# Optimization experiments

Measured on AMD Instinct MI355X. Metric: run time of the kernel, lower is better.

The kernel has to match this reference:

```python
import jax, jax.numpy as jnp
import numpy as np

B = 65536
G = 9          # grid_size
C = 10         # num_classes
BS = 3         # block_size = sqrt(grid_size)
CONSTRAINT_WEIGHT = 0.1


def setup_inputs() -> dict:
    key = jax.random.key(0)
    k1, k2, k3 = jax.random.split(key, 3)
    logits = jax.random.normal(k1, (B, G, G, C), dtype=jnp.float32)
    targets = jax.random.randint(k2, (B, G, G), 0, C)
    puzzles = jax.random.randint(k3, (B, G, G), 0, C)
    return {"logits": logits, "targets": targets, "puzzles": puzzles}


def _sudoku_loss(logits, targets, puzzles):
    mask = (puzzles == 0).astype(logits.dtype)               # [B, G, G]

    # --- masked cross-entropy over empty cells ---
    logp = jax.nn.log_softmax(logits, axis=-1)               # [B, G, G, C]
    ce = -jnp.take_along_axis(logp, targets[..., None], axis=-1)[..., 0]
    ce_loss = (ce * mask).sum() / (mask.sum() + 1e-8)

    # --- constraint loss (rows, cols, 3x3 boxes), fully vectorized ---
    probs = jnp.exp(logp)                                    # softmax probs
    wp = probs * mask[..., None]                             # [B, G, G, C]

    def group_mse(digit_sums, msum):
        # digit_sums: [B, G_groups, C]; msum: [B, G_groups]
        # torch: per-group F.mse_loss over [B, C-1], summed over groups
        target = msum[..., None] / G                         # [B, Gg, 1]
        diff = digit_sums[..., 1:] - target                  # [B, Gg, C-1]
        return (diff * diff).mean(axis=(0, 2)).sum()

    # rows: sum over columns (axis 2)
    row_loss = group_mse(wp.sum(axis=2), mask.sum(axis=2))
    # cols: sum over rows (axis 1)
    col_loss = group_mse(wp.sum(axis=1), mask.sum(axis=1))
    # boxes: reshape to [B, bi, ri, bj, cj, C], sum within-box dims
    box_ds = wp.reshape(B, BS, BS, BS, BS, C).sum(axis=(2, 4)).reshape(B, G, C)
    box_ms = mask.reshape(B, BS, BS, BS, BS).sum(axis=(2, 4)).reshape(B, G)
    box_loss = group_mse(box_ds, box_ms)

    num_constraints = G * 2 + BS * BS                        # 27
    constraint_loss = (row_loss + col_loss + box_loss) / num_constraints

    # torch wraps the constraint loss in torch.tensor(...), detaching it
    total = ce_loss + CONSTRAINT_WEIGHT * jax.lax.stop_gradient(constraint_loss)
    return total, ce_loss, constraint_loss


def reference(logits, targets, puzzles):
    total, ce_loss, constraint_loss = _sudoku_loss(logits, targets, puzzles)
    return total, ce_loss, constraint_loss
```

## Files before the change

kernel.cpp:

```cpp
#include <hip/hip_runtime.h>


constexpr int kB = 65536;
constexpr int kPuzzPerBlk = 3;
constexpr int kBlocks = (kB + kPuzzPerBlk - 1) / kPuzzPerBlk;

__global__ __launch_bounds__(256) void sudoku_main(
    const float* __restrict__ logits,
    const int*   __restrict__ targets,
    const int*   __restrict__ puzzles,
    float*       __restrict__ ws)
{
    __shared__ float acc[kPuzzPerBlk][27][10];
    __shared__ float red[4][3];

    const int tid = threadIdx.x;
    for (int i = tid; i < kPuzzPerBlk * 270; i += 256) ((float*)acc)[i] = 0.f;
    __syncthreads();

    float ce = 0.f, mcnt = 0.f, diff2 = 0.f;

    const int q    = tid / 81;
    const int cell = tid - q * 81;
    const int p    = blockIdx.x * kPuzzPerBlk + q;
    const bool valid = (tid < 243) && (p < kB);

    if (valid) {
        const size_t base = (size_t)p * 81 + cell;
        const int pz = puzzles[base];
        if (pz == 0) {
            const int t = targets[base];
            const float* xp = logits + base * 10;
            float x[10];
            #pragma unroll
            for (int h = 0; h < 5; ++h) {
                const float2 v = *(const float2*)(xp + 2 * h);
                x[2 * h] = v.x; x[2 * h + 1] = v.y;
            }
            float mx = x[0];
            #pragma unroll
            for (int c = 1; c < 10; ++c) mx = fmaxf(mx, x[c]);
            float e[10], S = 0.f;
            #pragma unroll
            for (int c = 0; c < 10; ++c) { e[c] = __expf(x[c] - mx); S += e[c]; }
            const float inv = 1.f / S;
            const float lse = __logf(S);

            float xt = x[0];
            #pragma unroll
            for (int c = 1; c < 10; ++c) xt = (t == c) ? x[c] : xt;
            ce   += mx + lse - xt;
            mcnt += 1.f;

            const int r  = cell / 9;
            const int cj = cell - r * 9;
            const int bx = (r / 3) * 3 + (cj / 3);
            float* rowa = acc[q][r];
            float* cola = acc[q][9 + cj];
            float* boxa = acc[q][18 + bx];
            atomicAdd(&rowa[0], 1.f);
            atomicAdd(&cola[0], 1.f);
            atomicAdd(&boxa[0], 1.f);
            #pragma unroll
            for (int c = 1; c < 10; ++c) {
                const float w = e[c] * inv;
                atomicAdd(&rowa[c], w);
                atomicAdd(&cola[c], w);
                atomicAdd(&boxa[c], w);
            }
        }
    }
    __syncthreads();

    if (tid < kPuzzPerBlk * 27) {
        const int q2 = tid / 27;
        const int g  = tid - q2 * 27;
        if (blockIdx.x * kPuzzPerBlk + q2 < kB) {
            const float* a = acc[q2][g];
            const float tg = a[0] * (1.f / 9.f);
            #pragma unroll
            for (int c = 1; c < 10; ++c) { const float d = a[c] - tg; diff2 += d * d; }
        }
    }

    #pragma unroll
    for (int off = 32; off > 0; off >>= 1) {
        diff2 += __shfl_down(diff2, off);
        ce    += __shfl_down(ce, off);
        mcnt  += __shfl_down(mcnt, off);
    }
    const int wave = tid >> 6;
    const int lane = tid & 63;
    if (lane == 0) { red[wave][0] = diff2; red[wave][1] = ce; red[wave][2] = mcnt; }
    __syncthreads();
    if (tid == 0) {
        float d = 0.f, c2 = 0.f, m = 0.f;
        #pragma unroll
        for (int wv = 0; wv < 4; ++wv) { d += red[wv][0]; c2 += red[wv][1]; m += red[wv][2]; }
        const int b = blockIdx.x;
        ws[b]               = d;
        ws[kBlocks + b]     = c2;
        ws[2 * kBlocks + b] = m;
    }
}

__global__ __launch_bounds__(1024) void sudoku_final(
    const float* __restrict__ ws, float* __restrict__ out)
{
    __shared__ float red[16][3];
    float s0 = 0.f, s1 = 0.f, s2 = 0.f;
    for (int i = threadIdx.x; i < kBlocks; i += 1024) {
        s0 += ws[i];
        s1 += ws[kBlocks + i];
        s2 += ws[2 * kBlocks + i];
    }
    #pragma unroll
    for (int off = 32; off > 0; off >>= 1) {
        s0 += __shfl_down(s0, off);
        s1 += __shfl_down(s1, off);
        s2 += __shfl_down(s2, off);
    }
    const int wave = threadIdx.x >> 6;
    if ((threadIdx.x & 63) == 0) { red[wave][0] = s0; red[wave][1] = s1; red[wave][2] = s2; }
    __syncthreads();
    if (threadIdx.x == 0) {
        float d = 0.f, c2 = 0.f, m = 0.f;
        #pragma unroll
        for (int wv = 0; wv < 16; ++wv) { d += red[wv][0]; c2 += red[wv][1]; m += red[wv][2]; }
        const float ce_loss    = c2 / (m + 1e-8f);
        const float constraint = d / ((float)kB * 9.f * 27.f);
        out[0] = ce_loss + 0.1f * constraint;
        out[1] = ce_loss;
        out[2] = constraint;
    }
}

extern "C" void kernel_launch(void* const* d_in, const int* in_sizes, int n_in,
                              void* d_out, int out_size, void* d_ws, size_t ws_size,
                              hipStream_t stream)
{
    const float* logits  = (const float*)d_in[0];
    const int*   targets = (const int*)d_in[1];
    const int*   puzzles = (const int*)d_in[2];
    float* ws  = (float*)d_ws;
    float* out = (float*)d_out;

    sudoku_main<<<kBlocks, 256, 0, stream>>>(logits, targets, puzzles, ws);
    sudoku_final<<<1, 1024, 0, stream>>>(ws, out);
}
```

Measured before the change: 369.1 us.

## Persistent tiled blocks with coalesced staging and masked-cell compaction

Replaces one-block-per-3-puzzles with 1024 persistent blocks that each loop over 8-puzzle tiles. Puzzles and targets are staged into shared memory with int4 loads, and logits are copied with float4 loads only where an empty cell is touched. Each wave builds a ballot-compacted worklist of empty cells so lanes stay busy. This aims to cut uncoalesced float2 global reads and skip loading logits for filled cells, at the cost of more barriers per tile and extra shared-memory traffic.

```diff
diff --git a/kernel.cpp b/kernel.cpp
--- a/kernel.cpp
+++ b/kernel.cpp
@@ -1,9 +1,13 @@
 #include <hip/hip_runtime.h>
 
 
-constexpr int kB = 65536;
-constexpr int kPuzzPerBlk = 3;
-constexpr int kBlocks = (kB + kPuzzPerBlk - 1) / kPuzzPerBlk;
+constexpr int kB            = 65536;
+constexpr int kPuzzPerTile  = 8;
+constexpr int kCellsPerTile = kPuzzPerTile * 81;
+constexpr int kFloatsPerTile= kCellsPerTile * 10;
+constexpr int kVec4PerTile  = kFloatsPerTile / 4;
+constexpr int kBlocks       = 1024;
+constexpr int kTilesPerBlk  = kB / (kBlocks * kPuzzPerTile);
 
 __global__ __launch_bounds__(256) void sudoku_main(
     const float* __restrict__ logits,
@@ -11,26 +15,64 @@
     const int*   __restrict__ puzzles,
     float*       __restrict__ ws)
 {
-    __shared__ float acc[kPuzzPerBlk][27][10];
-    __shared__ float red[4][3];
+    __shared__ float         lgs[kFloatsPerTile];
+    __shared__ unsigned char pzs[kCellsPerTile];
+    __shared__ int           tgs[kCellsPerTile];
+    __shared__ float         acc[kPuzzPerTile][27][10];
+    __shared__ unsigned short wl[4][164];
+    __shared__ float         red[4][3];
 
-    const int tid = threadIdx.x;
-    for (int i = tid; i < kPuzzPerBlk * 270; i += 256) ((float*)acc)[i] = 0.f;
-    __syncthreads();
+    const int tid  = threadIdx.x;
+    const int wave = tid >> 6;
+    const int lane = tid & 63;
 
-    float ce = 0.f, mcnt = 0.f, diff2 = 0.f;
+    for (int i = tid; i < kPuzzPerTile * 270; i += 256) ((float*)acc)[i] = 0.f;
 
-    const int q    = tid / 81;
-    const int cell = tid - q * 81;
-    const int p    = blockIdx.x * kPuzzPerBlk + q;
-    const bool valid = (tid < 243) && (p < kB);
+    float diff2 = 0.f, ce = 0.f, mcnt = 0.f;
 
-    if (valid) {
-        const size_t base = (size_t)p * 81 + cell;
-        const int pz = puzzles[base];
-        if (pz == 0) {
-            const int t = targets[base];
-            const float* xp = logits + base * 10;
+    for (int it = 0; it < kTilesPerBlk; ++it) {
+        const size_t tile     = (size_t)blockIdx.x * kTilesPerBlk + it;
+        const size_t cellBase = tile * kCellsPerTile;
+
+        if (tid < kCellsPerTile / 4) {
+            const int4 v = ((const int4*)(puzzles + cellBase))[tid];
+            unsigned char* p = &pzs[4 * tid];
+            p[0] = (unsigned char)v.x; p[1] = (unsigned char)v.y;
+            p[2] = (unsigned char)v.z; p[3] = (unsigned char)v.w;
+            ((int4*)tgs)[tid] = ((const int4*)(targets + cellBase))[tid];
+        }
+        __syncthreads();
+
+        {
+            const float4* lg4 = (const float4*)(logits + cellBase * 10);
+            #pragma unroll
+            for (int k = tid; k < kVec4PerTile; k += 256) {
+                const int f0 = 4 * k;
+                const int c0 = f0 / 10;
+                const int c1 = (f0 + 3) / 10;
+                if ((pzs[c0] == 0) || (pzs[c1] == 0))
+                    ((float4*)lgs)[k] = lg4[k];
+            }
+        }
+
+        int wcount = 0;
+        {
+            const int wbase = wave * 162;
+            #pragma unroll
+            for (int rb = 0; rb < 162; rb += 64) {
+                const int ci = rb + lane;
+                const bool m = (ci < 162) && (pzs[wbase + ci] == 0);
+                const unsigned long long bal = __ballot(m);
+                const int pre = __popcll(bal & ((1ULL << lane) - 1ULL));
+                if (m) wl[wave][wcount + pre] = (unsigned short)(wbase + ci);
+                wcount += (int)__popcll(bal);
+            }
+        }
+        __syncthreads();
+
+        for (int i = lane; i < wcount; i += 64) {
+            const int cid = wl[wave][i];
+            const float* xp = &lgs[cid * 10];
             float x[10];
             #pragma unroll
             for (int h = 0; h < 5; ++h) {
@@ -46,18 +88,22 @@
             const float inv = 1.f / S;
             const float lse = __logf(S);
 
+            const int t = tgs[cid];
             float xt = x[0];
             #pragma unroll
             for (int c = 1; c < 10; ++c) xt = (t == c) ? x[c] : xt;
             ce   += mx + lse - xt;
             mcnt += 1.f;
 
-            const int r  = cell / 9;
-            const int cj = cell - r * 9;
-            const int bx = (r / 3) * 3 + (cj / 3);
-            float* rowa = acc[q][r];
-            float* cola = acc[q][9 + cj];
-            float* boxa = acc[q][18 + bx];
+            const int q    = cid / 81;
+            const int cell = cid - q * 81;
+            const int r    = cell / 9;
+            const int cj   = cell - r * 9;
+            const int bx   = (r / 3) * 3 + (cj / 3);
+            float* A = &acc[q][0][0];
+            float* rowa = A + r * 10;
+            float* cola = A + (9 + cj) * 10;
+            float* boxa = A + (18 + bx) * 10;
             atomicAdd(&rowa[0], 1.f);
             atomicAdd(&cola[0], 1.f);
             atomicAdd(&boxa[0], 1.f);
@@ -69,18 +115,19 @@
                 atomicAdd(&boxa[c], w);
             }
         }
-    }
-    __syncthreads();
+        __syncthreads();
 
-    if (tid < kPuzzPerBlk * 27) {
-        const int q2 = tid / 27;
-        const int g  = tid - q2 * 27;
-        if (blockIdx.x * kPuzzPerBlk + q2 < kB) {
-            const float* a = acc[q2][g];
+        if (tid < kPuzzPerTile * 27) {
+            const int q = tid / 27;
+            const int g = tid - q * 27;
+            float* a = &acc[q][g][0];
             const float tg = a[0] * (1.f / 9.f);
             #pragma unroll
             for (int c = 1; c < 10; ++c) { const float d = a[c] - tg; diff2 += d * d; }
+            #pragma unroll
+            for (int c = 0; c < 10; ++c) a[c] = 0.f;
         }
+        __syncthreads();
     }
 
     #pragma unroll
@@ -89,8 +136,6 @@
         ce    += __shfl_down(ce, off);
         mcnt  += __shfl_down(mcnt, off);
     }
-    const int wave = tid >> 6;
-    const int lane = tid & 63;
     if (lane == 0) { red[wave][0] = diff2; red[wave][1] = ce; red[wave][2] = mcnt; }
     __syncthreads();
     if (tid == 0) {
@@ -98,18 +143,18 @@
         #pragma unroll
         for (int wv = 0; wv < 4; ++wv) { d += red[wv][0]; c2 += red[wv][1]; m += red[wv][2]; }
         const int b = blockIdx.x;
-        ws[b]               = d;
-        ws[kBlocks + b]     = c2;
-        ws[2 * kBlocks + b] = m;
+        ws[b]                = d;
+        ws[kBlocks + b]      = c2;
+        ws[2 * kBlocks + b]  = m;
     }
 }
 
-__global__ __launch_bounds__(1024) void sudoku_final(
+__global__ __launch_bounds__(256) void sudoku_final(
     const float* __restrict__ ws, float* __restrict__ out)
 {
-    __shared__ float red[16][3];
+    __shared__ float red[4][3];
     float s0 = 0.f, s1 = 0.f, s2 = 0.f;
-    for (int i = threadIdx.x; i < kBlocks; i += 1024) {
+    for (int i = threadIdx.x; i < kBlocks; i += 256) {
         s0 += ws[i];
         s1 += ws[kBlocks + i];
         s2 += ws[2 * kBlocks + i];
@@ -126,7 +171,7 @@
     if (threadIdx.x == 0) {
         float d = 0.f, c2 = 0.f, m = 0.f;
         #pragma unroll
-        for (int wv = 0; wv < 16; ++wv) { d += red[wv][0]; c2 += red[wv][1]; m += red[wv][2]; }
+        for (int wv = 0; wv < 4; ++wv) { d += red[wv][0]; c2 += red[wv][1]; m += red[wv][2]; }
         const float ce_loss    = c2 / (m + 1e-8f);
         const float constraint = d / ((float)kB * 9.f * 27.f);
         out[0] = ce_loss + 0.1f * constraint;
@@ -146,5 +191,5 @@
     float* out = (float*)d_out;
 
     sudoku_main<<<kBlocks, 256, 0, stream>>>(logits, targets, puzzles, ws);
-    sudoku_final<<<1, 1024, 0, stream>>>(ws, out);
+    sudoku_final<<<1, 256, 0, stream>>>(ws, out);
 }
```

Result: slower. 380.8 us (+3.2%).

## Restructure main kernel into per-wave staged loop with float4 loads and register prefetch

Applied to the files above, without the earlier changes.

Each wave now processes 16 puzzles in 8 stages, loading logits as coalesced float4 into per-wave LDS while prefetching the next stage into registers. Block-level barriers are removed in favor of wave-private accumulators, and per-wave partials are written for a smaller final reduction. This targets poor memory coalescing and sync overhead of the one-thread-per-cell layout, at the cost of fewer resident waves and reliance on wave-synchronous LDS semantics without barriers.

```diff
diff --git a/kernel.cpp b/kernel.cpp
--- a/kernel.cpp
+++ b/kernel.cpp
@@ -1,9 +1,15 @@
 #include <hip/hip_runtime.h>
 
 
-constexpr int kB = 65536;
-constexpr int kPuzzPerBlk = 3;
-constexpr int kBlocks = (kB + kPuzzPerBlk - 1) / kPuzzPerBlk;
+constexpr int kB             = 65536;
+constexpr int kBlocks        = 1024;
+constexpr int kWavesPerBlk   = 4;
+constexpr int kWaves         = kBlocks * kWavesPerBlk;
+constexpr int kStages        = 8;
+constexpr int kPuzzPerStage  = 2;
+constexpr int kCellsPerStage = kPuzzPerStage * 81;
+constexpr int kVec4PerStage  = kCellsPerStage * 10 / 4;
+constexpr int kAccFloats     = kPuzzPerStage * 27 * 10;
 
 __global__ __launch_bounds__(256) void sudoku_main(
     const float* __restrict__ logits,
@@ -11,75 +17,129 @@
     const int*   __restrict__ puzzles,
     float*       __restrict__ ws)
 {
-    __shared__ float acc[kPuzzPerBlk][27][10];
-    __shared__ float red[4][3];
-
-    const int tid = threadIdx.x;
-    for (int i = tid; i < kPuzzPerBlk * 270; i += 256) ((float*)acc)[i] = 0.f;
-    __syncthreads();
-
-    float ce = 0.f, mcnt = 0.f, diff2 = 0.f;
-
-    const int q    = tid / 81;
-    const int cell = tid - q * 81;
-    const int p    = blockIdx.x * kPuzzPerBlk + q;
-    const bool valid = (tid < 243) && (p < kB);
-
-    if (valid) {
-        const size_t base = (size_t)p * 81 + cell;
-        const int pz = puzzles[base];
-        if (pz == 0) {
-            const int t = targets[base];
-            const float* xp = logits + base * 10;
-            float x[10];
-            #pragma unroll
-            for (int h = 0; h < 5; ++h) {
-                const float2 v = *(const float2*)(xp + 2 * h);
-                x[2 * h] = v.x; x[2 * h + 1] = v.y;
+    __shared__ float lgs[kWavesPerBlk][kVec4PerStage * 4];
+    __shared__ float accs[kWavesPerBlk][kAccFloats];
+
+    const int tid  = threadIdx.x;
+    const int wave = tid >> 6;
+    const int lane = tid & 63;
+    float* Lg = lgs[wave];
+    float* Ac = accs[wave];
+
+    for (int i = lane; i < kAccFloats; i += 64) Ac[i] = 0.f;
+
+    const int wgid = blockIdx.x * kWavesPerBlk + wave;
+    const size_t puzz0 = (size_t)wgid * (kStages * kPuzzPerStage);
+    const float4* lgbase = (const float4*)(logits + puzz0 * 810);
+    const int*    pzbase = puzzles + puzz0 * 81;
+    const int*    tgbase = targets + puzz0 * 81;
+
+    float4 nxt[7];
+    int pzn[3], tgn[3];
+    #pragma unroll
+    for (int k = 0; k < 7; ++k) {
+        const int v = 64 * k + lane;
+        if (v < kVec4PerStage) nxt[k] = lgbase[v];
+    }
+    #pragma unroll
+    for (int k = 0; k < 3; ++k) {
+        const int c = 64 * k + lane;
+        if (c < kCellsPerStage) { pzn[k] = pzbase[c]; tgn[k] = tgbase[c]; }
+    }
+
+    float diff2 = 0.f, ce = 0.f, mcnt = 0.f;
+
+    #pragma unroll 2
+    for (int s = 0; s < kStages; ++s) {
+        float4 cur[7];
+        int pzc[3], tgc[3];
+        #pragma unroll
+        for (int k = 0; k < 7; ++k) cur[k] = nxt[k];
+        #pragma unroll
+        for (int k = 0; k < 3; ++k) { pzc[k] = pzn[k]; tgc[k] = tgn[k]; }
+
+        #pragma unroll
+        for (int k = 0; k < 7; ++k) {
+            const int v = 64 * k + lane;
+            if (v < kVec4PerStage) ((float4*)Lg)[v] = cur[k];
+        }
+
+        if (s + 1 < kStages) {
+            const float4* nb  = lgbase + (size_t)(s + 1) * kVec4PerStage;
+            const int*    npz = pzbase + (s + 1) * kCellsPerStage;
+            const int*    ntg = tgbase + (s + 1) * kCellsPerStage;
+            #pragma unroll
+            for (int k = 0; k < 7; ++k) {
+                const int v = 64 * k + lane;
+                if (v < kVec4PerStage) nxt[k] = nb[v];
             }
-            float mx = x[0];
-            #pragma unroll
-            for (int c = 1; c < 10; ++c) mx = fmaxf(mx, x[c]);
-            float e[10], S = 0.f;
-            #pragma unroll
-            for (int c = 0; c < 10; ++c) { e[c] = __expf(x[c] - mx); S += e[c]; }
-            const float inv = 1.f / S;
-            const float lse = __logf(S);
-
-            float xt = x[0];
-            #pragma unroll
-            for (int c = 1; c < 10; ++c) xt = (t == c) ? x[c] : xt;
-            ce   += mx + lse - xt;
-            mcnt += 1.f;
-
-            const int r  = cell / 9;
-            const int cj = cell - r * 9;
-            const int bx = (r / 3) * 3 + (cj / 3);
-            float* rowa = acc[q][r];
-            float* cola = acc[q][9 + cj];
-            float* boxa = acc[q][18 + bx];
-            atomicAdd(&rowa[0], 1.f);
-            atomicAdd(&cola[0], 1.f);
-            atomicAdd(&boxa[0], 1.f);
-            #pragma unroll
-            for (int c = 1; c < 10; ++c) {
-                const float w = e[c] * inv;
-                atomicAdd(&rowa[c], w);
-                atomicAdd(&cola[c], w);
-                atomicAdd(&boxa[c], w);
+            #pragma unroll
+            for (int k = 0; k < 3; ++k) {
+                const int c = 64 * k + lane;
+                if (c < kCellsPerStage) { pzn[k] = npz[c]; tgn[k] = ntg[c]; }
             }
         }
-    }
-    __syncthreads();
-
-    if (tid < kPuzzPerBlk * 27) {
-        const int q2 = tid / 27;
-        const int g  = tid - q2 * 27;
-        if (blockIdx.x * kPuzzPerBlk + q2 < kB) {
-            const float* a = acc[q2][g];
-            const float tg = a[0] * (1.f / 9.f);
-            #pragma unroll
-            for (int c = 1; c < 10; ++c) { const float d = a[c] - tg; diff2 += d * d; }
+
+        #pragma unroll
+        for (int k = 0; k < 3; ++k) {
+            const int c = 64 * k + lane;
+            if (c < kCellsPerStage) {
+                const float* xp = Lg + c * 10;
+                float x[10];
+                #pragma unroll
+                for (int h = 0; h < 5; ++h) {
+                    const float2 v = *(const float2*)(xp + 2 * h);
+                    x[2 * h] = v.x; x[2 * h + 1] = v.y;
+                }
+                float mx = x[0];
+                #pragma unroll
+                for (int cc = 1; cc < 10; ++cc) mx = fmaxf(mx, x[cc]);
+                float e[10], S = 0.f;
+                #pragma unroll
+                for (int cc = 0; cc < 10; ++cc) { e[cc] = __expf(x[cc] - mx); S += e[cc]; }
+                const float inv = 1.f / S;
+                const float lse = __logf(S);
+
+                const int pz = pzc[k];
+                const int t  = tgc[k];
+                float xt = x[0];
+                #pragma unroll
+                for (int cc = 1; cc < 10; ++cc) xt = (t == cc) ? x[cc] : xt;
+                const float maskf = (pz == 0) ? 1.f : 0.f;
+                ce   += maskf * (mx + lse - xt);
+                mcnt += maskf;
+
+                if (pz == 0) {
+                    const int q   = c / 81;
+                    const int c81 = c - 81 * q;
+                    const int r   = c81 / 9;
+                    const int cj  = c81 - 9 * r;
+                    const int bx  = (r / 3) * 3 + (cj / 3);
+                    float* A    = Ac + q * 270;
+                    float* rowa = A + r * 10;
+                    float* cola = A + (9 + cj) * 10;
+                    float* boxa = A + (18 + bx) * 10;
+                    atomicAdd(&rowa[0], 1.f);
+                    atomicAdd(&cola[0], 1.f);
+                    atomicAdd(&boxa[0], 1.f);
+                    #pragma unroll
+                    for (int cc = 1; cc < 10; ++cc) {
+                        const float w = e[cc] * inv;
+                        atomicAdd(&rowa[cc], w);
+                        atomicAdd(&cola[cc], w);
+                        atomicAdd(&boxa[cc], w);
+                    }
+                }
+            }
+        }
+
+        if (lane < kPuzzPerStage * 27) {
+            float* a = Ac + lane * 10;
+            const float tg9 = a[0] * (1.f / 9.f);
+            #pragma unroll
+            for (int cc = 1; cc < 10; ++cc) { const float d = a[cc] - tg9; diff2 += d * d; }
+            #pragma unroll
+            for (int cc = 0; cc < 10; ++cc) a[cc] = 0.f;
         }
     }
 
@@ -89,30 +149,22 @@
         ce    += __shfl_down(ce, off);
         mcnt  += __shfl_down(mcnt, off);
     }
-    const int wave = tid >> 6;
-    const int lane = tid & 63;
-    if (lane == 0) { red[wave][0] = diff2; red[wave][1] = ce; red[wave][2] = mcnt; }
-    __syncthreads();
-    if (tid == 0) {
-        float d = 0.f, c2 = 0.f, m = 0.f;
-        #pragma unroll
-        for (int wv = 0; wv < 4; ++wv) { d += red[wv][0]; c2 += red[wv][1]; m += red[wv][2]; }
-        const int b = blockIdx.x;
-        ws[b]               = d;
-        ws[kBlocks + b]     = c2;
-        ws[2 * kBlocks + b] = m;
+    if (lane == 0) {
+        ws[wgid]              = diff2;
+        ws[kWaves + wgid]     = ce;
+        ws[2 * kWaves + wgid] = mcnt;
     }
 }
 
-__global__ __launch_bounds__(1024) void sudoku_final(
+__global__ __launch_bounds__(256) void sudoku_final(
     const float* __restrict__ ws, float* __restrict__ out)
 {
-    __shared__ float red[16][3];
+    __shared__ float red[4][3];
     float s0 = 0.f, s1 = 0.f, s2 = 0.f;
-    for (int i = threadIdx.x; i < kBlocks; i += 1024) {
+    for (int i = threadIdx.x; i < kWaves; i += 256) {
         s0 += ws[i];
-        s1 += ws[kBlocks + i];
-        s2 += ws[2 * kBlocks + i];
+        s1 += ws[kWaves + i];
+        s2 += ws[2 * kWaves + i];
     }
     #pragma unroll
     for (int off = 32; off > 0; off >>= 1) {
@@ -126,7 +178,7 @@
     if (threadIdx.x == 0) {
         float d = 0.f, c2 = 0.f, m = 0.f;
         #pragma unroll
-        for (int wv = 0; wv < 16; ++wv) { d += red[wv][0]; c2 += red[wv][1]; m += red[wv][2]; }
+        for (int wv = 0; wv < 4; ++wv) { d += red[wv][0]; c2 += red[wv][1]; m += red[wv][2]; }
         const float ce_loss    = c2 / (m + 1e-8f);
         const float constraint = d / ((float)kB * 9.f * 27.f);
         out[0] = ce_loss + 0.1f * constraint;
@@ -146,5 +198,5 @@
     float* out = (float*)d_out;
 
     sudoku_main<<<kBlocks, 256, 0, stream>>>(logits, targets, puzzles, ws);
-    sudoku_final<<<1, 1024, 0, stream>>>(ws, out);
+    sudoku_final<<<1, 256, 0, stream>>>(ws, out);
 }
```

Result: no change. 374.7 us (+1.5%).
